# Optimization experiments

Hardware: AMD Instinct MI355X
Metric: run time of the kernel (lower is better)

The kernel has to match this reference:

```python
import jax, jax.numpy as jnp
import numpy as np

H = 16  # num_attention_heads


def setup_inputs() -> dict:
    key = jax.random.key(0)
    k1, k2, k3 = jax.random.split(key, 3)
    B, S, E = 2, 2048, 1024
    return {
        "hidden_states": jax.random.normal(k1, (B, S, E), dtype=jnp.float32),
        "W_attn": jax.random.normal(k2, (E, 3 * E), dtype=jnp.float32) * 0.02,
        "b_attn": jnp.zeros((3 * E,), dtype=jnp.float32),
        "W_proj": jax.random.normal(k3, (E, E), dtype=jnp.float32) * 0.02,
        "b_proj": jnp.zeros((E,), dtype=jnp.float32),
    }


def reference(hidden_states, W_attn, b_attn, W_proj, b_proj):
    B, S, E = hidden_states.shape
    hd = E // H
    # Conv1D: x @ W + b -> [B, S, 3E]
    qkv = hidden_states @ W_attn + b_attn
    # Faithful to module: _split_heads with 3*head_dim FIRST, then split q/k/v.
    # i.e. per-head slice of size 3*hd is [q_h | k_h | v_h] (interleaved layout).
    qkv = qkv.reshape(B, S, H, 3 * hd).transpose(0, 2, 1, 3)  # [B, H, S, 3*hd]
    q, k, v = jnp.split(qkv, 3, axis=-1)                      # each [B, H, S, hd]
    # scores, scaled by sqrt(head_dim) (value.size(-1) ** 0.5)
    scores = jnp.einsum("bhqd,bhkd->bhqk", q, k) / jnp.asarray(hd, q.dtype) ** 0.5
    # causal mask via where with masked_bias = -10000.0 (not -inf), as in module
    causal = jnp.tril(jnp.ones((S, S), dtype=bool))
    scores = jnp.where(causal, scores, jnp.asarray(-10000.0, scores.dtype))
    attn_weights = jax.nn.softmax(scores, axis=-1)  # dropout p=0 -> identity
    attn_out = jnp.einsum("bhqk,bhkd->bhqd", attn_weights, v)
    attn_out = attn_out.transpose(0, 2, 1, 3).reshape(B, S, E)  # merge heads
    return attn_out @ W_proj + b_proj
```

## Files before the change

### kernel.cpp

```cpp
#include <hip/hip_runtime.h>
#include <hip/hip_bf16.h>


typedef __attribute__((ext_vector_type(4))) float f32x4;
typedef __attribute__((ext_vector_type(8))) short short8;

#define AS1 __attribute__((address_space(1)))
#define AS3 __attribute__((address_space(3)))

__device__ __forceinline__ void load_lds16(const void* g, void* l) {
    __builtin_amdgcn_global_load_lds((const AS1 void*)g, (AS3 void*)l, 16, 0, 0);
}

__device__ __forceinline__ unsigned short f2bf(float f) {
    union { float f; unsigned int u; } v; v.f = f;
    unsigned int r = v.u + 0x7FFFu + ((v.u >> 16) & 1u);
    return (unsigned short)(r >> 16);
}

template <int CTRL>
__device__ __forceinline__ float rot_add(float x) {
    int r = __builtin_amdgcn_update_dpp(0, __builtin_bit_cast(int, x), CTRL, 0xF, 0xF, false);
    return x + __builtin_bit_cast(float, r);
}

__device__ __forceinline__ void transpose_tile(
    const float* __restrict__ W, unsigned short* __restrict__ Wt,
    int K, int N, int bx, int by, int t) {
    __shared__ float tile[32][33];
    int k0 = by * 32, n0 = bx * 32;
    int r = t >> 3, c = (t & 7) * 4;
    float4 v = *(const float4*)&W[(size_t)(k0 + r) * N + n0 + c];
    tile[r][c] = v.x; tile[r][c + 1] = v.y; tile[r][c + 2] = v.z; tile[r][c + 3] = v.w;
    __syncthreads();
    int n = t >> 3; int kk = (t & 7) * 4;
    ushort4 o;
    o.x = f2bf(tile[kk + 0][n]);
    o.y = f2bf(tile[kk + 1][n]);
    o.z = f2bf(tile[kk + 2][n]);
    o.w = f2bf(tile[kk + 3][n]);
    *(ushort4*)&Wt[(size_t)(n0 + n) * K + k0 + kk] = o;
}

__global__ __launch_bounds__(256) void prep(
    const float* __restrict__ hs, unsigned short* __restrict__ Xb,
    const float* __restrict__ W_attn, unsigned short* __restrict__ WaT,
    const float* __restrict__ W_proj, unsigned short* __restrict__ WpT) {
    int bid = blockIdx.x, t = threadIdx.x;
    if (bid < 4096) {
        int i = (bid * 256 + t) * 4;
        float4 v = *(const float4*)(hs + i);
        ushort4 o;
        o.x = f2bf(v.x); o.y = f2bf(v.y); o.z = f2bf(v.z); o.w = f2bf(v.w);
        *(ushort4*)(Xb + i) = o;
    } else if (bid < 7168) {
        int r = bid - 4096;
        transpose_tile(W_attn, WaT, 1024, 3072, r % 96, r / 96, t);
    } else {
        int r = bid - 7168;
        transpose_tile(W_proj, WpT, 1024, 1024, r % 32, r / 32, t);
    }
}

__global__ __launch_bounds__(256) void gemm_qkv(
    const unsigned short* __restrict__ A,
    const unsigned short* __restrict__ Bt,
    const float* __restrict__ bias,
    unsigned short* __restrict__ qk, unsigned short* __restrict__ Vt,
    int M, int N, int K) {
    __shared__ unsigned short Sh[8704];
    unsigned short* As = Sh;
    unsigned short* Bs = Sh + 4096;
    unsigned short* Tb = Sh;
    const int t = threadIdx.x, wave = t >> 6, lane = t & 63;
    const int l15 = lane & 15, quad = lane >> 4;
    const int m0 = blockIdx.y * 128, n0 = blockIdx.x * 128;
    const int srow = wave * 32 + (lane >> 2);
    const int sch = (lane & 3) * 8;
    const unsigned short* Ag = A + (size_t)(m0 + srow) * K + sch;
    const unsigned short* Bg = Bt + (size_t)(n0 + srow) * K + sch;
    unsigned short* AsW = &As[wave * 32 * 32];
    unsigned short* BsW = &Bs[wave * 32 * 32];
    const int wm = (wave >> 1) * 64, wn = (wave & 1) * 64;
    f32x4 acc[4][4] = {};
    for (int k0 = 0; k0 < K; k0 += 32) {
        load_lds16(Ag + k0, AsW);
        load_lds16(Ag + k0 + (size_t)16 * K, AsW + 16 * 32);
        load_lds16(Bg + k0, BsW);
        load_lds16(Bg + k0 + (size_t)16 * K, BsW + 16 * 32);
        __syncthreads();
        short8 af[4], bf[4];
#pragma unroll
        for (int i = 0; i < 4; ++i) {
            af[i] = *(const short8*)&As[(wm + i * 16 + l15) * 32 + quad * 8];
            bf[i] = *(const short8*)&Bs[(wn + i * 16 + l15) * 32 + quad * 8];
        }
#pragma unroll
        for (int mt = 0; mt < 4; ++mt)
#pragma unroll
            for (int nt = 0; nt < 4; ++nt)
                acc[mt][nt] = __builtin_amdgcn_mfma_f32_16x16x32_bf16(af[mt], bf[nt], acc[mt][nt], 0, 0, 0);
        __syncthreads();
    }
    const int rem = n0 % 192;
#pragma unroll
    for (int mt = 0; mt < 4; ++mt) {
        int mrow = m0 + wm + mt * 16 + quad * 4;
#pragma unroll
        for (int nt = 0; nt < 4; ++nt) {
            int col = n0 + wn + nt * 16 + l15;
            float bv = bias[col];
            int h = col / 192;
            int j = col - h * 192;
            if (j < 128) {
#pragma unroll
                for (int r = 0; r < 4; ++r)
                    qk[(size_t)(mrow + r) * 2048 + h * 128 + j] = f2bf(acc[mt][nt][r] + bv);
            } else {
                int d = j - 128;
                int s_local = wm + mt * 16 + quad * 4;
                ushort4 pk;
                pk.x = f2bf(acc[mt][nt][0] + bv);
                pk.y = f2bf(acc[mt][nt][1] + bv);
                pk.z = f2bf(acc[mt][nt][2] + bv);
                pk.w = f2bf(acc[mt][nt][3] + bv);
                *(ushort4*)&Tb[d * 136 + s_local] = pk;
            }
        }
    }
    if (rem != 0) {
        __syncthreads();
        int vhalf = (rem == 64) ? 1 : 0;
        int h = (n0 + vhalf * 64) / 192;
        int b = m0 >> 11;
        unsigned short* vbase = Vt + ((size_t)(b * 16 + h) * 64) * 2048 + (m0 & 2047);
        int drow = t >> 4, ch = (t & 15) * 8;
#pragma unroll
        for (int rr = 0; rr < 4; ++rr) {
            int d = rr * 16 + drow;
            *(uint4*)(vbase + (size_t)d * 2048 + ch) = *(const uint4*)&Tb[d * 136 + ch];
        }
    }
}

__global__ __launch_bounds__(256) void gemm_proj(
    const unsigned short* __restrict__ A,
    const unsigned short* __restrict__ Bt,
    const float* __restrict__ bias,
    float* __restrict__ C, int M, int N, int K) {
    __shared__ unsigned short As[128 * 32];
    __shared__ unsigned short Bs[64 * 32];
    const int t = threadIdx.x, wave = t >> 6, lane = t & 63;
    const int l15 = lane & 15, quad = lane >> 4;
    const int m0 = blockIdx.y * 128, n0 = blockIdx.x * 64;
    const int srowA = wave * 32 + (lane >> 2);
    const int sch = (lane & 3) * 8;
    const unsigned short* Ag = A + (size_t)(m0 + srowA) * K + sch;
    const unsigned short* Bg = Bt + (size_t)(n0 + wave * 16 + (lane >> 2)) * K + sch;
    unsigned short* AsW = &As[wave * 32 * 32];
    unsigned short* BsW = &Bs[wave * 16 * 32];
    const int wm = (wave >> 1) * 64, wn = (wave & 1) * 32;
    f32x4 acc[4][2] = {};
    for (int k0 = 0; k0 < K; k0 += 32) {
        load_lds16(Ag + k0, AsW);
        load_lds16(Ag + k0 + (size_t)16 * K, AsW + 16 * 32);
        load_lds16(Bg + k0, BsW);
        __syncthreads();
        short8 af[4], bf[2];
#pragma unroll
        for (int i = 0; i < 4; ++i)
            af[i] = *(const short8*)&As[(wm + i * 16 + l15) * 32 + quad * 8];
#pragma unroll
        for (int i = 0; i < 2; ++i)
            bf[i] = *(const short8*)&Bs[(wn + i * 16 + l15) * 32 + quad * 8];
#pragma unroll
        for (int mt = 0; mt < 4; ++mt)
#pragma unroll
            for (int nt = 0; nt < 2; ++nt)
                acc[mt][nt] = __builtin_amdgcn_mfma_f32_16x16x32_bf16(af[mt], bf[nt], acc[mt][nt], 0, 0, 0);
        __syncthreads();
    }
#pragma unroll
    for (int mt = 0; mt < 4; ++mt) {
        int mrow = m0 + wm + mt * 16 + quad * 4;
#pragma unroll
        for (int nt = 0; nt < 2; ++nt) {
            int col = n0 + wn + nt * 16 + l15;
            float bv = bias[col];
#pragma unroll
            for (int r = 0; r < 4; ++r)
                C[(size_t)(mrow + r) * N + col] = acc[mt][nt][r] + bv;
        }
    }
}

__device__ __forceinline__ void attn_tile(
    f32x4 (&o)[4], float (&lrun)[4],
    const short8 (&qf)[2],
    const unsigned short (*Ks)[72], const unsigned short (*Vts)[72],
    unsigned short (*Psw)[72],
    bool diag, int wave, int l15, int quad) {
    f32x4 s[4] = {};
#pragma unroll
    for (int km = 0; km < 2; ++km)
#pragma unroll
        for (int nt = 0; nt < 4; ++nt) {
            short8 kf = *(const short8*)&Ks[nt * 16 + l15][km * 32 + quad * 8];
            s[nt] = __builtin_amdgcn_mfma_f32_16x16x32_bf16(qf[km], kf, s[nt], 0, 0, 0);
        }
    float lt[4] = {0.f, 0.f, 0.f, 0.f};
#pragma unroll
    for (int nt = 0; nt < 4; ++nt)
#pragma unroll
        for (int r = 0; r < 4; ++r) {
            float v = s[nt][r] * 0.125f;
            if (diag && (nt * 16 + l15 > wave * 16 + quad * 4 + r)) v = -10000.0f;
            float pv = __expf(v);
            lt[r] += pv;
            Psw[quad * 4 + r][nt * 16 + l15] = f2bf(pv);
        }
#pragma unroll
    for (int r = 0; r < 4; ++r) {
        float v = lt[r];
        v = rot_add<0x121>(v); v = rot_add<0x122>(v);
        v = rot_add<0x124>(v); v = rot_add<0x128>(v);
        lrun[r] += v;
    }
#pragma unroll
    for (int km = 0; km < 2; ++km) {
        short8 pf = *(const short8*)&Psw[l15][km * 32 + quad * 8];
#pragma unroll
        for (int nt = 0; nt < 4; ++nt) {
            short8 vf = *(const short8*)&Vts[nt * 16 + l15][km * 32 + quad * 8];
            o[nt] = __builtin_amdgcn_mfma_f32_16x16x32_bf16(pf, vf, o[nt], 0, 0, 0);
        }
    }
}

__global__ __launch_bounds__(256) void attn1(
    const unsigned short* __restrict__ qk,
    const unsigned short* __restrict__ Vt,
    unsigned short* __restrict__ out) {
    const int S = 2048;
    __shared__ unsigned short Ks[64][72];
    __shared__ unsigned short Vts[64][72];
    __shared__ unsigned short Ps[4][16][72];
    int t = threadIdx.x, wave = t >> 6, lane = t & 63;
    int l15 = lane & 15, quad = lane >> 4;
    int bid = blockIdx.x;
    int qt = 31 - (bid >> 5);
    int bh = bid & 31;
    int b = bh >> 4, h = bh & 15;
    const unsigned short* qkb = qk + (size_t)b * S * 2048 + h * 128;
    const unsigned short* vtb = Vt + (size_t)bh * 64 * 2048;

    short8 qf[2];
    {
        int qr = qt * 64 + wave * 16 + l15;
#pragma unroll
        for (int km = 0; km < 2; ++km)
            qf[km] = *(const short8*)(qkb + (size_t)qr * 2048 + km * 32 + quad * 8);
    }
    f32x4 o[4] = {};
    float lrun[4] = {0.f, 0.f, 0.f, 0.f};

    int srow8 = t >> 3, chunk8 = (t & 7) * 8;
    int vd = t >> 2, vch = (t & 3) * 8;

    uint4 kreg0, kreg1, vreg0, vreg1;
    {
        kreg0 = *(const uint4*)(qkb + (size_t)(srow8) * 2048 + 64 + chunk8);
        kreg1 = *(const uint4*)(qkb + (size_t)(32 + srow8) * 2048 + 64 + chunk8);
        const unsigned short* vsrc = vtb + (size_t)vd * 2048;
        vreg0 = *(const uint4*)(vsrc + vch);
        vreg1 = *(const uint4*)(vsrc + vch + 32);
    }

    for (int kt = 0; kt <= qt; ++kt) {
        __syncthreads();
        *(uint4*)&Ks[srow8][chunk8] = kreg0;
        *(uint4*)&Ks[32 + srow8][chunk8] = kreg1;
        *(uint4*)&Vts[vd][vch] = vreg0;
        *(uint4*)&Vts[vd][vch + 32] = vreg1;
        __syncthreads();
        if (kt < qt) {
            int kn = kt + 1;
            kreg0 = *(const uint4*)(qkb + (size_t)(kn * 64 + srow8) * 2048 + 64 + chunk8);
            kreg1 = *(const uint4*)(qkb + (size_t)(kn * 64 + 32 + srow8) * 2048 + 64 + chunk8);
            const unsigned short* vsrc = vtb + (size_t)vd * 2048 + kn * 64;
            vreg0 = *(const uint4*)(vsrc + vch);
            vreg1 = *(const uint4*)(vsrc + vch + 32);
        }
        attn_tile(o, lrun, qf, Ks, Vts, Ps[wave], kt == qt, wave, l15, quad);
    }
    unsigned short* ob = out + (size_t)b * S * 1024 + h * 64;
#pragma unroll
    for (int r = 0; r < 4; ++r) {
        float inv = 1.0f / lrun[r];
        int srow = qt * 64 + wave * 16 + quad * 4 + r;
#pragma unroll
        for (int nt = 0; nt < 4; ++nt)
            ob[(size_t)srow * 1024 + nt * 16 + l15] = f2bf(o[nt][r] * inv);
    }
}

extern "C" void kernel_launch(void* const* d_in, const int* in_sizes, int n_in,
                              void* d_out, int out_size, void* d_ws, size_t ws_size,
                              hipStream_t stream) {
    const float* hs     = (const float*)d_in[0];
    const float* W_attn = (const float*)d_in[1];
    const float* b_attn = (const float*)d_in[2];
    const float* W_proj = (const float*)d_in[3];
    const float* b_proj = (const float*)d_in[4];
    float* out = (float*)d_out;

    const int B = 2, S = 2048, E = 1024;
    const int M = B * S;
    const int N3 = 3 * E;

    unsigned short* Xb  = (unsigned short*)d_ws;
    unsigned short* WaT = Xb + (size_t)M * E;
    unsigned short* WpT = WaT + (size_t)N3 * E;
    unsigned short* qkb = WpT + (size_t)E * E;
    unsigned short* Vt  = qkb + (size_t)M * 2048;
    unsigned short* ao  = Vt + (size_t)M * E;

    prep<<<dim3(8192), 256, 0, stream>>>(hs, Xb, W_attn, WaT, W_proj, WpT);

    gemm_qkv<<<dim3(N3 / 128, M / 128), 256, 0, stream>>>(Xb, WaT, b_attn, qkb, Vt, M, N3, E);

    attn1<<<dim3(32 * 32), 256, 0, stream>>>(qkb, Vt, ao);

    gemm_proj<<<dim3(E / 64, M / 128), 256, 0, stream>>>(ao, WpT, b_proj, out, M, E, E);
}
```

Before: 191.2 us.

## Rewrite attention kernel with 128-row query tiles and register-resident P

The attention kernel now gives each wave 32 query rows instead of 16, so every K/V tile staged in LDS serves twice as many queries, and the grid shrinks to 512 blocks in a balanced causal order. The scores are computed as S^T so P can be packed to bf16 in registers and rearranged with permlane32_swap and ds_swizzle, which removes the LDS round trip for P. The 1/sqrt(d) scale is folded into Q inside the QKV GEMM epilogue, the row-sum reduction is deferred until after the loop, and MFMA sections run at raised wave priority. Register pressure rises, and fewer blocks may reduce occupancy.

```diff
diff --git a/kernel.cpp b/kernel.cpp
--- a/kernel.cpp
+++ b/kernel.cpp
@@ -4,6 +4,7 @@
 
 typedef __attribute__((ext_vector_type(4))) float f32x4;
 typedef __attribute__((ext_vector_type(8))) short short8;
+typedef __attribute__((ext_vector_type(2))) unsigned int uint2v;
 
 #define AS1 __attribute__((address_space(1)))
 #define AS3 __attribute__((address_space(3)))
@@ -18,10 +19,10 @@
     return (unsigned short)(r >> 16);
 }
 
-template <int CTRL>
-__device__ __forceinline__ float rot_add(float x) {
-    int r = __builtin_amdgcn_update_dpp(0, __builtin_bit_cast(int, x), CTRL, 0xF, 0xF, false);
-    return x + __builtin_bit_cast(float, r);
+__device__ __forceinline__ int cvt_pk_bf16(float lo, float hi) {
+    int r;
+    asm("v_cvt_pk_bf16_f32 %0, %1, %2" : "=v"(r) : "v"(lo), "v"(hi));
+    return r;
 }
 
 __device__ __forceinline__ void transpose_tile(
@@ -113,9 +114,10 @@
             int h = col / 192;
             int j = col - h * 192;
             if (j < 128) {
+                float sc = (j < 64) ? 0.125f : 1.0f;
 #pragma unroll
                 for (int r = 0; r < 4; ++r)
-                    qk[(size_t)(mrow + r) * 2048 + h * 128 + j] = f2bf(acc[mt][nt][r] + bv);
+                    qk[(size_t)(mrow + r) * 2048 + h * 128 + j] = f2bf((acc[mt][nt][r] + bv) * sc);
             } else {
                 int d = j - 128;
                 int s_local = wm + mt * 16 + quad * 4;
@@ -194,113 +196,156 @@
     }
 }
 
-__device__ __forceinline__ void attn_tile(
-    f32x4 (&o)[4], float (&lrun)[4],
-    const short8 (&qf)[2],
-    const unsigned short (*Ks)[72], const unsigned short (*Vts)[72],
-    unsigned short (*Psw)[72],
-    bool diag, int wave, int l15, int quad) {
-    f32x4 s[4] = {};
-#pragma unroll
-    for (int km = 0; km < 2; ++km)
-#pragma unroll
-        for (int nt = 0; nt < 4; ++nt) {
-            short8 kf = *(const short8*)&Ks[nt * 16 + l15][km * 32 + quad * 8];
-            s[nt] = __builtin_amdgcn_mfma_f32_16x16x32_bf16(qf[km], kf, s[nt], 0, 0, 0);
-        }
-    float lt[4] = {0.f, 0.f, 0.f, 0.f};
-#pragma unroll
-    for (int nt = 0; nt < 4; ++nt)
-#pragma unroll
-        for (int r = 0; r < 4; ++r) {
-            float v = s[nt][r] * 0.125f;
-            if (diag && (nt * 16 + l15 > wave * 16 + quad * 4 + r)) v = -10000.0f;
-            float pv = __expf(v);
-            lt[r] += pv;
-            Psw[quad * 4 + r][nt * 16 + l15] = f2bf(pv);
-        }
-#pragma unroll
-    for (int r = 0; r < 4; ++r) {
-        float v = lt[r];
-        v = rot_add<0x121>(v); v = rot_add<0x122>(v);
-        v = rot_add<0x124>(v); v = rot_add<0x128>(v);
-        lrun[r] += v;
-    }
+__device__ __forceinline__ void build_af(const int (&pk)[4][2], int qpar, short8 (&af)[2]) {
 #pragma unroll
     for (int km = 0; km < 2; ++km) {
-        short8 pf = *(const short8*)&Psw[l15][km * 32 + quad * 8];
-#pragma unroll
-        for (int nt = 0; nt < 4; ++nt) {
-            short8 vf = *(const short8*)&Vts[nt * 16 + l15][km * 32 + quad * 8];
-            o[nt] = __builtin_amdgcn_mfma_f32_16x16x32_bf16(pf, vf, o[nt], 0, 0, 0);
-        }
-    }
-}
-
-__global__ __launch_bounds__(256) void attn1(
+        uint2v r0 = __builtin_amdgcn_permlane32_swap(
+            (unsigned)pk[2 * km][0], (unsigned)pk[2 * km + 1][0], false, false);
+        uint2v r1 = __builtin_amdgcn_permlane32_swap(
+            (unsigned)pk[2 * km][1], (unsigned)pk[2 * km + 1][1], false, false);
+        int Ap0 = (int)r0[0], Bp0 = (int)r0[1];
+        int Ap1 = (int)r1[0], Bp1 = (int)r1[1];
+        int z0 = qpar ? Ap0 : Bp0;
+        int z1 = qpar ? Ap1 : Bp1;
+        int w0 = __builtin_amdgcn_ds_swizzle(z0, 0x401F);
+        int w1 = __builtin_amdgcn_ds_swizzle(z1, 0x401F);
+        int f0 = qpar ? w0 : Ap0, f1 = qpar ? w1 : Ap1;
+        int g0 = qpar ? Bp0 : w0, g1 = qpar ? Bp1 : w1;
+        int4 v = {f0, f1, g0, g1};
+        af[km] = __builtin_bit_cast(short8, v);
+    }
+}
+
+__global__ __launch_bounds__(256) void attn2(
     const unsigned short* __restrict__ qk,
     const unsigned short* __restrict__ Vt,
     unsigned short* __restrict__ out) {
     const int S = 2048;
     __shared__ unsigned short Ks[64][72];
     __shared__ unsigned short Vts[64][72];
-    __shared__ unsigned short Ps[4][16][72];
-    int t = threadIdx.x, wave = t >> 6, lane = t & 63;
-    int l15 = lane & 15, quad = lane >> 4;
-    int bid = blockIdx.x;
-    int qt = 31 - (bid >> 5);
-    int bh = bid & 31;
-    int b = bh >> 4, h = bh & 15;
+    const int t = threadIdx.x, wave = t >> 6, lane = t & 63;
+    const int l15 = lane & 15, quad = lane >> 4, qpar = quad & 1;
+    const int bid = blockIdx.x;
+    const int qt = (bid < 256) ? (15 - (bid >> 5)) : ((bid - 256) >> 5);
+    const int bh = bid & 31;
+    const int b = bh >> 4, h = bh & 15;
     const unsigned short* qkb = qk + (size_t)b * S * 2048 + h * 128;
     const unsigned short* vtb = Vt + (size_t)bh * 64 * 2048;
 
-    short8 qf[2];
-    {
-        int qr = qt * 64 + wave * 16 + l15;
+    const int q0 = qt * 128 + wave * 32;
+    short8 qf[2][2];
+#pragma unroll
+    for (int sp = 0; sp < 2; ++sp) {
+        int qr = q0 + sp * 16 + l15;
 #pragma unroll
         for (int km = 0; km < 2; ++km)
-            qf[km] = *(const short8*)(qkb + (size_t)qr * 2048 + km * 32 + quad * 8);
-    }
-    f32x4 o[4] = {};
-    float lrun[4] = {0.f, 0.f, 0.f, 0.f};
-
-    int srow8 = t >> 3, chunk8 = (t & 7) * 8;
-    int vd = t >> 2, vch = (t & 3) * 8;
-
-    uint4 kreg0, kreg1, vreg0, vreg1;
-    {
-        kreg0 = *(const uint4*)(qkb + (size_t)(srow8) * 2048 + 64 + chunk8);
-        kreg1 = *(const uint4*)(qkb + (size_t)(32 + srow8) * 2048 + 64 + chunk8);
-        const unsigned short* vsrc = vtb + (size_t)vd * 2048;
-        vreg0 = *(const uint4*)(vsrc + vch);
-        vreg1 = *(const uint4*)(vsrc + vch + 32);
-    }
-
-    for (int kt = 0; kt <= qt; ++kt) {
+            qf[sp][km] = *(const short8*)(qkb + (size_t)qr * 2048 + km * 32 + quad * 8);
+    }
+    f32x4 o0[4] = {}, o1[4] = {};
+    float lr0 = 0.f, lr1 = 0.f;
+
+    const int srow8 = t >> 3, chunk8 = (t & 7) * 8;
+    const int vd = t >> 2, vch = (t & 3) * 8;
+    const int KT = qt * 2 + 2;
+
+    uint4 kreg0 = *(const uint4*)(qkb + (size_t)srow8 * 2048 + 64 + chunk8);
+    uint4 kreg1 = *(const uint4*)(qkb + (size_t)(32 + srow8) * 2048 + 64 + chunk8);
+    uint4 vreg0 = *(const uint4*)(vtb + (size_t)vd * 2048 + vch);
+    uint4 vreg1 = *(const uint4*)(vtb + (size_t)vd * 2048 + vch + 32);
+
+    const int qg0 = q0 + l15, qg1 = q0 + 16 + l15;
+    const int q1max = q0 + 31;
+
+    for (int kt = 0; kt < KT; ++kt) {
         __syncthreads();
         *(uint4*)&Ks[srow8][chunk8] = kreg0;
         *(uint4*)&Ks[32 + srow8][chunk8] = kreg1;
         *(uint4*)&Vts[vd][vch] = vreg0;
         *(uint4*)&Vts[vd][vch + 32] = vreg1;
         __syncthreads();
-        if (kt < qt) {
-            int kn = kt + 1;
-            kreg0 = *(const uint4*)(qkb + (size_t)(kn * 64 + srow8) * 2048 + 64 + chunk8);
-            kreg1 = *(const uint4*)(qkb + (size_t)(kn * 64 + 32 + srow8) * 2048 + 64 + chunk8);
-            const unsigned short* vsrc = vtb + (size_t)vd * 2048 + kn * 64;
-            vreg0 = *(const uint4*)(vsrc + vch);
-            vreg1 = *(const uint4*)(vsrc + vch + 32);
-        }
-        attn_tile(o, lrun, qf, Ks, Vts, Ps[wave], kt == qt, wave, l15, quad);
-    }
+        if (kt + 1 < KT) {
+            int kn = (kt + 1) * 64;
+            kreg0 = *(const uint4*)(qkb + (size_t)(kn + srow8) * 2048 + 64 + chunk8);
+            kreg1 = *(const uint4*)(qkb + (size_t)(kn + 32 + srow8) * 2048 + 64 + chunk8);
+            vreg0 = *(const uint4*)(vtb + (size_t)vd * 2048 + kn + vch);
+            vreg1 = *(const uint4*)(vtb + (size_t)vd * 2048 + kn + vch + 32);
+        }
+        const int kb = kt * 64;
+        if (kb > q1max) continue;
+
+        f32x4 s0[4] = {}, s1[4] = {};
+        __builtin_amdgcn_s_setprio(1);
+#pragma unroll
+        for (int km = 0; km < 2; ++km)
+#pragma unroll
+            for (int nt = 0; nt < 4; ++nt) {
+                short8 kf = *(const short8*)&Ks[nt * 16 + l15][km * 32 + quad * 8];
+                s0[nt] = __builtin_amdgcn_mfma_f32_16x16x32_bf16(kf, qf[0][km], s0[nt], 0, 0, 0);
+                s1[nt] = __builtin_amdgcn_mfma_f32_16x16x32_bf16(kf, qf[1][km], s1[nt], 0, 0, 0);
+            }
+        __builtin_amdgcn_s_setprio(0);
+
+        const int ka = kb + quad * 4;
+        if (kb + 63 > q0) {
+#pragma unroll
+            for (int nt = 0; nt < 4; ++nt)
+#pragma unroll
+                for (int r = 0; r < 4; ++r) {
+                    if (ka + nt * 16 + r > qg0) s0[nt][r] = -1e30f;
+                    if (ka + nt * 16 + r > qg1) s1[nt][r] = -1e30f;
+                }
+        }
+
+        int pk0[4][2], pk1[4][2];
+        float a0 = 0.f, a1 = 0.f;
+#pragma unroll
+        for (int nt = 0; nt < 4; ++nt) {
+            float pa[4], pb[4];
+#pragma unroll
+            for (int r = 0; r < 4; ++r) {
+                pa[r] = __expf(s0[nt][r]);
+                pb[r] = __expf(s1[nt][r]);
+                a0 += pa[r]; a1 += pb[r];
+            }
+            pk0[nt][0] = cvt_pk_bf16(pa[0], pa[1]);
+            pk0[nt][1] = cvt_pk_bf16(pa[2], pa[3]);
+            pk1[nt][0] = cvt_pk_bf16(pb[0], pb[1]);
+            pk1[nt][1] = cvt_pk_bf16(pb[2], pb[3]);
+        }
+        lr0 += a0; lr1 += a1;
+
+        short8 af0[2], af1[2];
+        build_af(pk0, qpar, af0);
+        build_af(pk1, qpar, af1);
+
+        __builtin_amdgcn_s_setprio(1);
+#pragma unroll
+        for (int km = 0; km < 2; ++km)
+#pragma unroll
+            for (int nt = 0; nt < 4; ++nt) {
+                short8 vf = *(const short8*)&Vts[nt * 16 + l15][km * 32 + quad * 8];
+                o0[nt] = __builtin_amdgcn_mfma_f32_16x16x32_bf16(af0[km], vf, o0[nt], 0, 0, 0);
+                o1[nt] = __builtin_amdgcn_mfma_f32_16x16x32_bf16(af1[km], vf, o1[nt], 0, 0, 0);
+            }
+        __builtin_amdgcn_s_setprio(0);
+    }
+
+    float t0 = lr0 + __shfl_xor(lr0, 16);
+    t0 += __shfl_xor(t0, 32);
+    float t1 = lr1 + __shfl_xor(lr1, 16);
+    t1 += __shfl_xor(t1, 32);
     unsigned short* ob = out + (size_t)b * S * 1024 + h * 64;
 #pragma unroll
     for (int r = 0; r < 4; ++r) {
-        float inv = 1.0f / lrun[r];
-        int srow = qt * 64 + wave * 16 + quad * 4 + r;
-#pragma unroll
-        for (int nt = 0; nt < 4; ++nt)
-            ob[(size_t)srow * 1024 + nt * 16 + l15] = f2bf(o[nt][r] * inv);
+        float i0 = 1.0f / __shfl(t0, quad * 4 + r);
+        float i1 = 1.0f / __shfl(t1, quad * 4 + r);
+        size_t r0 = (size_t)(q0 + quad * 4 + r) * 1024;
+        size_t r1 = (size_t)(q0 + 16 + quad * 4 + r) * 1024;
+#pragma unroll
+        for (int nt = 0; nt < 4; ++nt) {
+            ob[r0 + nt * 16 + l15] = f2bf(o0[nt][r] * i0);
+            ob[r1 + nt * 16 + l15] = f2bf(o1[nt][r] * i1);
+        }
     }
 }
 
@@ -329,7 +374,7 @@
 
     gemm_qkv<<<dim3(N3 / 128, M / 128), 256, 0, stream>>>(Xb, WaT, b_attn, qkb, Vt, M, N3, E);
 
-    attn1<<<dim3(32 * 32), 256, 0, stream>>>(qkb, Vt, ao);
+    attn2<<<dim3(512), 256, 0, stream>>>(qkb, Vt, ao);
 
     gemm_proj<<<dim3(E / 64, M / 128), 256, 0, stream>>>(ao, WpT, b_proj, out, M, E, E);
 }
```

Result: slower. 195.9 us (+2.5%).
